# Optimization experiments

Measured on AMD Instinct MI355X. Metric: run time of the kernel, lower is better.

Reference implementation:

```python
import jax, jax.numpy as jnp
import numpy as np

B, S, E, H = 2, 2048, 1024, 16
D = E // H


def setup_inputs() -> dict:
    key = jax.random.key(0)
    ks = jax.random.split(key, 8)
    q = jax.random.normal(ks[0], (B, S, E), dtype=jnp.float32)
    k = jax.random.normal(ks[1], (B, S, E), dtype=jnp.float32)
    v = jax.random.normal(ks[2], (B, S, E), dtype=jnp.float32)
    mask = jax.random.randint(ks[3], (B, 1, 1, S), 0, 2, dtype=jnp.int32)
    sc = 1.0 / np.sqrt(E)
    W_qkv = jax.random.normal(ks[4], (3 * E, E), dtype=jnp.float32) * sc
    b_qkv = jnp.zeros((3 * E,), dtype=jnp.float32)
    W_out = jax.random.normal(ks[5], (E, E), dtype=jnp.float32) * sc
    b_out = jnp.zeros((E,), dtype=jnp.float32)
    return {"q": q, "k": k, "v": v, "mask": mask,
            "W_qkv": W_qkv, "b_qkv": b_qkv, "W_out": W_out, "b_out": b_out}


def reference(q, k, v, mask, W_qkv, b_qkv, W_out, b_out):
    # Fused qkv linear: q takes the Q-slice, k the K-slice, v the V-slice.
    qp = (q @ W_qkv[:E].T + b_qkv[:E]).reshape(B, S, H, D)
    kp = (k @ W_qkv[E:2 * E].T + b_qkv[E:2 * E]).reshape(B, S, H, D)
    vp = (v @ W_qkv[2 * E:].T + b_qkv[2 * E:]).reshape(B, S, H, D)
    # (B,H,S,S) scores -- NOTE: original module does NOT scale by sqrt(d)
    energy = jnp.einsum('nqhd,nkhd->nhqk', qp, kp)
    energy = jnp.where(mask == 0, jnp.float32(-1e20), energy)
    attention = jax.nn.softmax(energy, axis=-1)
    out = jnp.einsum('nhql,nlhd->nqhd', attention, vp).reshape(B, S, E)
    return out @ W_out.T + b_out
```

## Files before the change

### kernel.cpp

```cpp
#include <hip/hip_runtime.h>
#include <stdint.h>

constexpr int B_ = 2, S_ = 2048, E_ = 1024, H_ = 16, D_ = 64;
constexpr int M_ = B_ * S_;

typedef unsigned short u16;
typedef __attribute__((ext_vector_type(8))) short short8;
typedef __attribute__((ext_vector_type(4))) float f32x4;

__device__ __forceinline__ u16 f2bf(float f) {
  uint32_t u = __float_as_uint(f);
  return (u16)((u + 0x7FFFu + ((u >> 16) & 1u)) >> 16);
}
__device__ __forceinline__ void tsplit(float x, u16& hi, u16& lo) {
  const uint32_t u = __float_as_uint(x);
  hi = (u16)(u >> 16);
  const float hif = __uint_as_float(u & 0xFFFF0000u);
  lo = (u16)(__float_as_uint(x - hif) >> 16);
}

__device__ __forceinline__ void block_sync() {
  asm volatile("s_waitcnt lgkmcnt(0)" ::: "memory");
  __builtin_amdgcn_s_barrier();
}

typedef const __attribute__((address_space(1))) unsigned int GU32;
typedef __attribute__((address_space(3))) unsigned int LU32;
__device__ __forceinline__ void gload16(const void* g, void* l) {
  __builtin_amdgcn_global_load_lds((GU32*)g, (LU32*)l, 16, 0, 0);
}

__global__ __launch_bounds__(256) void split_f32_kernel(
    const float* __restrict__ src, u16* __restrict__ hi, u16* __restrict__ lo, int n4)
{
  const int i = blockIdx.x * 256 + threadIdx.x;
  if (i >= n4) return;
  const float4 x = ((const float4*)src)[i];
  ushort4 h, l;
  tsplit(x.x, h.x, l.x); tsplit(x.y, h.y, l.y);
  tsplit(x.z, h.z, l.z); tsplit(x.w, h.w, l.w);
  ((ushort4*)hi)[i] = h;
  ((ushort4*)lo)[i] = l;
}

__global__ __launch_bounds__(256) void mask_scan_kernel(
    const int* __restrict__ mask, int* __restrict__ opos, int* __restrict__ nk)
{
  __shared__ int tmp[256];
  __shared__ int coff;
  const int b = blockIdx.x, t = threadIdx.x;
  for (int c = t; c < S_; c += 256) opos[b * S_ + c] = 0;
  if (t == 0) coff = 0;
  __syncthreads();
  for (int c = 0; c < S_; c += 256) {
    const int m = (mask[b * S_ + c + t] != 0) ? 1 : 0;
    int x = m;
    tmp[t] = x;
    __syncthreads();
#pragma unroll
    for (int off = 1; off < 256; off <<= 1) {
      const int v = (t >= off) ? tmp[t - off] : 0;
      __syncthreads();
      x += v;
      tmp[t] = x;
      __syncthreads();
    }
    const int base = coff;
    if (m) opos[b * S_ + base + x - 1] = c + t;
    __syncthreads();
    if (t == 255) coff = base + x;
    __syncthreads();
  }
  if (t == 0) nk[b] = coff;
}

__global__ __launch_bounds__(256) void gemm_qkv_kernel(
    const float* __restrict__ q, const float* __restrict__ k, const float* __restrict__ v,
    const u16* __restrict__ WHi, const u16* __restrict__ WLo,
    const float* __restrict__ bias,
    const int* __restrict__ Opos, const int* __restrict__ NkArr,
    u16* __restrict__ QpHi, u16* __restrict__ QpLo,
    u16* __restrict__ KpHi, u16* __restrict__ KpLo,
    u16* __restrict__ Vp)
{
  __shared__ __align__(16) short smem[18432];
  short* Ah = smem;
  short* Al = smem + 5120;
  short* Bh = smem + 10240;
  short* Bl = smem + 14336;

  const int t = threadIdx.x;
  const int m0 = blockIdx.x * 128;
  const int n0g = blockIdx.y * 128;
  const int proj = n0g >> 10;
  const int nloc = n0g & (E_ - 1);
  const bool split = (proj < 2);
  const int bb = m0 >> 11, mloc = m0 & (S_ - 1);
  const int nkb = NkArr[bb];
  if (proj != 0 && mloc >= nkb) return;

  const float* A = (proj == 0) ? q : (proj == 1) ? k : v;

  const int w = t >> 6, lane = t & 63;
  const int g = lane >> 4, lc = lane & 15;
  const int wm = w & 1, wn = w >> 1;
  const int sra = t >> 1, sca = (t & 1) * 16;

  int arow;
  if (proj == 0) arow = m0 + sra;
  else arow = bb * S_ + (Opos[bb * S_ + mloc + sra] & (S_ - 1));
  const float* Ab = A + (size_t)arow * E_ + sca;

  f32x4 acc[4][4];
#pragma unroll
  for (int i = 0; i < 4; ++i)
#pragma unroll
    for (int j = 0; j < 4; ++j) acc[i][j] = (f32x4){0.f, 0.f, 0.f, 0.f};

  auto loadA = [&](float4* a, int kk) {
#pragma unroll
    for (int i = 0; i < 4; ++i) a[i] = *(const float4*)(Ab + kk + 4 * i);
  };
  auto writeA = [&](const float4* a) {
    ushort hh[16], ll[16];
#pragma unroll
    for (int i = 0; i < 4; ++i) {
      tsplit(a[i].x, hh[4 * i + 0], ll[4 * i + 0]);
      tsplit(a[i].y, hh[4 * i + 1], ll[4 * i + 1]);
      tsplit(a[i].z, hh[4 * i + 2], ll[4 * i + 2]);
      tsplit(a[i].w, hh[4 * i + 3], ll[4 * i + 3]);
    }
    *(short8*)&Ah[sra * 40 + sca]     = *(const short8*)&hh[0];
    *(short8*)&Ah[sra * 40 + sca + 8] = *(const short8*)&hh[8];
    if (split) {
      *(short8*)&Al[sra * 40 + sca]     = *(const short8*)&ll[0];
      *(short8*)&Al[sra * 40 + sca + 8] = *(const short8*)&ll[8];
    }
  };
  auto gloadB = [&](int k0) {
#pragma unroll
    for (int i = 0; i < 2; ++i) {
      const int c = (w * 2 + i) * 64 + lane;
      const int row = c >> 2;
      const int sub = (c & 3) ^ ((row >> 1) & 3);
      const size_t go = (size_t)(n0g + row) * E_ + k0 + sub * 8;
      gload16(WHi + go, (char*)Bh + (w * 2 + i) * 1024);
      if (split) gload16(WLo + go, (char*)Bl + (w * 2 + i) * 1024);
    }
  };

  float4 ar[4];
  loadA(ar, 0);

  for (int k0 = 0; k0 < E_; k0 += 32) {
    __syncthreads();
    writeA(ar);
    gloadB(k0);
    __syncthreads();
    if (k0 + 32 < E_) loadA(ar, k0 + 32);

    short8 ah[4], al[4], bh[4], bl[4];
#pragma unroll
    for (int mt = 0; mt < 4; ++mt) {
      const int ro = (wm * 64 + mt * 16 + lc) * 40 + g * 8;
      ah[mt] = *(const short8*)&Ah[ro];
      if (split) al[mt] = *(const short8*)&Al[ro];
    }
#pragma unroll
    for (int nt = 0; nt < 4; ++nt) {
      const int row = wn * 64 + nt * 16 + lc;
      const int ro = row * 32 + ((g ^ ((row >> 1) & 3)) * 8);
      bh[nt] = *(const short8*)&Bh[ro];
      if (split) bl[nt] = *(const short8*)&Bl[ro];
    }
#pragma unroll
    for (int mt = 0; mt < 4; ++mt)
#pragma unroll
      for (int nt = 0; nt < 4; ++nt) {
        f32x4 a = acc[mt][nt];
        a = __builtin_amdgcn_mfma_f32_16x16x32_bf16(ah[mt], bh[nt], a, 0, 0, 0);
        if (split) {
          a = __builtin_amdgcn_mfma_f32_16x16x32_bf16(ah[mt], bl[nt], a, 0, 0, 0);
          a = __builtin_amdgcn_mfma_f32_16x16x32_bf16(al[mt], bh[nt], a, 0, 0, 0);
        }
        acc[mt][nt] = a;
      }
  }

  float bs[4];
#pragma unroll
  for (int nt = 0; nt < 4; ++nt) bs[nt] = bias[n0g + wn * 64 + nt * 16 + lc];

  if (proj < 2) {
    u16* Hi = (proj == 0) ? QpHi : KpHi;
    u16* Lo = (proj == 0) ? QpLo : KpLo;
    const int hwave = (nloc + wn * 64) >> 6;
    short* T = smem + w * 4608;
    const int srow_out = (proj == 0) ? ((m0 + wm * 64 + lane) & (S_ - 1))
                                     : (mloc + wm * 64 + lane);
    const size_t rowb = (((size_t)(bb * H_ + hwave)) * S_ + srow_out) * D_;
#pragma unroll
    for (int pass = 0; pass < 2; ++pass) {
      __syncthreads();
#pragma unroll
      for (int nt = 0; nt < 4; ++nt)
#pragma unroll
        for (int mt = 0; mt < 4; ++mt)
#pragma unroll
          for (int r = 0; r < 4; ++r) {
            const float val = acc[mt][nt][r] + bs[nt];
            const uint32_t u = __float_as_uint(val);
            u16 x;
            if (pass == 0) x = (u16)(u >> 16);
            else {
              const float hif = __uint_as_float(u & 0xFFFF0000u);
              x = (u16)(__float_as_uint(val - hif) >> 16);
            }
            T[(mt * 16 + g * 4 + r) * 72 + nt * 16 + lc] = (short)x;
          }
      __syncthreads();
      u16* dst = (pass == 0) ? Hi : Lo;
#pragma unroll
      for (int j = 0; j < 8; ++j)
        *(short8*)&dst[rowb + 8 * j] = *(const short8*)&T[lane * 72 + 8 * j];
    }
  } else {
#pragma unroll
    for (int mt = 0; mt < 4; ++mt) {
      const int jb = mloc + wm * 64 + mt * 16 + g * 4;
#pragma unroll
      for (int nt = 0; nt < 4; ++nt) {
        const int nE = nloc + wn * 64 + nt * 16 + lc;
        const int h = nE >> 6, d = nE & 63;
        const size_t rb = (((size_t)(bb * H_ + h)) * D_ + d) * S_;
#pragma unroll
        for (int r = 0; r < 4; ++r) {
          if (jb + r < nkb) Vp[rb + jb + r] = f2bf(acc[mt][nt][r] + bs[nt]);
        }
      }
    }
  }
}

__global__ __launch_bounds__(256, 4) void attn_mfma_kernel(
    const u16* __restrict__ QpHi, const u16* __restrict__ QpLo,
    const u16* __restrict__ KpHi, const u16* __restrict__ KpLo,
    const u16* __restrict__ Vp,
    const int* __restrict__ nkArr,
    u16* __restrict__ AOHi)
{
  __shared__ __align__(16) short sm[18432];
  short* Khi = sm;
  short* Klo = sm + 4608;
  short* Vt  = sm + 9216;
  short* Pb  = sm + 13824;

  const int t = threadIdx.x;
  const int w = t >> 6, lane = t & 63;
  const int g = lane >> 4, lc = lane & 15;
  const int bh = blockIdx.y;
  const int b = bh >> 4, hh = bh & 15;
  const int q0 = blockIdx.x * 64;
  const size_t hb = (size_t)bh * S_ * D_;
  const u16* QgH = QpHi + hb;
  const u16* QgL = QpLo + hb;
  const u16* KgH = KpHi + hb;
  const u16* KgL = KpLo + hb;
  const u16* Vg  = Vp + hb;
  short* Pw = Pb + w * 1152;

  const int nk = nkArr[b];
  const int kend = ((nk + 63) >> 6) << 6;

  short8 qh[2], ql[2];
  {
    const size_t base = (size_t)(q0 + 16 * w + lc) * D_ + 8 * g;
    qh[0] = *(const short8*)&QgH[base];
    qh[1] = *(const short8*)&QgH[base + 32];
    ql[0] = *(const short8*)&QgL[base];
    ql[1] = *(const short8*)&QgL[base + 32];
  }

  short8 ones8 = {0, 0, 0, 0, 0, 0, 0, 0};
  if (lc == 0) {
    const short o = (short)0x3F80;
    ones8 = (short8){o, o, o, o, o, o, o, o};
  }

  f32x4 O[4];
  f32x4 Ol = (f32x4){0.f, 0.f, 0.f, 0.f};
#pragma unroll
  for (int dt = 0; dt < 4; ++dt) O[dt] = (f32x4){0.f, 0.f, 0.f, 0.f};
  float mst[4] = {-INFINITY, -INFINITY, -INFINITY, -INFINITY};

  const int srow = t >> 2, sc16 = (t & 3) * 16;

  short8 kr[2], lr[2], vr[2];
  kr[0] = *(const short8*)&KgH[srow * D_ + sc16];
  kr[1] = *(const short8*)&KgH[srow * D_ + sc16 + 8];
  lr[0] = *(const short8*)&KgL[srow * D_ + sc16];
  lr[1] = *(const short8*)&KgL[srow * D_ + sc16 + 8];
  vr[0] = *(const short8*)&Vg[srow * S_ + sc16];
  vr[1] = *(const short8*)&Vg[srow * S_ + sc16 + 8];

  for (int kt = 0; kt < kend; kt += 64) {
    block_sync();
    *(short8*)&Khi[srow * 72 + sc16]     = kr[0];
    *(short8*)&Khi[srow * 72 + sc16 + 8] = kr[1];
    *(short8*)&Klo[srow * 72 + sc16]     = lr[0];
    *(short8*)&Klo[srow * 72 + sc16 + 8] = lr[1];
    *(short8*)&Vt[srow * 72 + sc16]      = vr[0];
    *(short8*)&Vt[srow * 72 + sc16 + 8]  = vr[1];
    block_sync();
    if (kt + 64 < kend) {
      const int kn = kt + 64;
      kr[0] = *(const short8*)&KgH[(kn + srow) * D_ + sc16];
      kr[1] = *(const short8*)&KgH[(kn + srow) * D_ + sc16 + 8];
      lr[0] = *(const short8*)&KgL[(kn + srow) * D_ + sc16];
      lr[1] = *(const short8*)&KgL[(kn + srow) * D_ + sc16 + 8];
      vr[0] = *(const short8*)&Vg[srow * S_ + kn + sc16];
      vr[1] = *(const short8*)&Vg[srow * S_ + kn + sc16 + 8];
    }

    f32x4 sc[4];
#pragma unroll
    for (int kt16 = 0; kt16 < 4; ++kt16) {
      const int ko = (16 * kt16 + lc) * 72 + 8 * g;
      const short8 kh0 = *(const short8*)&Khi[ko];
      const short8 kh1 = *(const short8*)&Khi[ko + 32];
      const short8 kl0 = *(const short8*)&Klo[ko];
      const short8 kl1 = *(const short8*)&Klo[ko + 32];
      f32x4 a = {0.f, 0.f, 0.f, 0.f};
      a = __builtin_amdgcn_mfma_f32_16x16x32_bf16(qh[0], kh0, a, 0, 0, 0);
      a = __builtin_amdgcn_mfma_f32_16x16x32_bf16(qh[1], kh1, a, 0, 0, 0);
      a = __builtin_amdgcn_mfma_f32_16x16x32_bf16(qh[0], kl0, a, 0, 0, 0);
      a = __builtin_amdgcn_mfma_f32_16x16x32_bf16(qh[1], kl1, a, 0, 0, 0);
      a = __builtin_amdgcn_mfma_f32_16x16x32_bf16(ql[0], kh0, a, 0, 0, 0);
      a = __builtin_amdgcn_mfma_f32_16x16x32_bf16(ql[1], kh1, a, 0, 0, 0);
      sc[kt16] = a;
    }

    if (kt + 64 > nk) {
#pragma unroll
      for (int kt16 = 0; kt16 < 4; ++kt16) {
        if (kt + 16 * kt16 + lc >= nk) {
          sc[kt16][0] = -1e20f; sc[kt16][1] = -1e20f;
          sc[kt16][2] = -1e20f; sc[kt16][3] = -1e20f;
        }
      }
    }

    float al[4];
#pragma unroll
    for (int r = 0; r < 4; ++r) {
      float vv = fmaxf(fmaxf(sc[0][r], sc[1][r]), fmaxf(sc[2][r], sc[3][r]));
      vv = fmaxf(vv, __shfl_xor(vv, 1));
      vv = fmaxf(vv, __shfl_xor(vv, 2));
      vv = fmaxf(vv, __shfl_xor(vv, 4));
      vv = fmaxf(vv, __shfl_xor(vv, 8));
      const float mn = fmaxf(mst[r], vv);
      al[r] = __expf(mst[r] - mn);
      mst[r] = mn;
    }
#pragma unroll
    for (int kt16 = 0; kt16 < 4; ++kt16) {
#pragma unroll
      for (int r = 0; r < 4; ++r)
        sc[kt16][r] = __expf(sc[kt16][r] - mst[r]);
    }
    const f32x4 alv = {al[0], al[1], al[2], al[3]};
    O[0] *= alv; O[1] *= alv; O[2] *= alv; O[3] *= alv;
    Ol *= alv;
#pragma unroll
    for (int kt16 = 0; kt16 < 4; ++kt16) {
#pragma unroll
      for (int r = 0; r < 4; ++r)
        Pw[(4 * g + r) * 72 + 16 * kt16 + lc] = (short)f2bf(sc[kt16][r]);
    }

    short8 pa[2];
    pa[0] = *(const short8*)&Pw[lc * 72 + 8 * g];
    pa[1] = *(const short8*)&Pw[lc * 72 + 32 + 8 * g];
    Ol = __builtin_amdgcn_mfma_f32_16x16x32_bf16(pa[0], ones8, Ol, 0, 0, 0);
    Ol = __builtin_amdgcn_mfma_f32_16x16x32_bf16(pa[1], ones8, Ol, 0, 0, 0);
#pragma unroll
    for (int dt = 0; dt < 4; ++dt) {
      const int vo = (16 * dt + lc) * 72 + 8 * g;
      const short8 vb0 = *(const short8*)&Vt[vo];
      const short8 vb1 = *(const short8*)&Vt[vo + 32];
      O[dt] = __builtin_amdgcn_mfma_f32_16x16x32_bf16(pa[0], vb0, O[dt], 0, 0, 0);
      O[dt] = __builtin_amdgcn_mfma_f32_16x16x32_bf16(pa[1], vb1, O[dt], 0, 0, 0);
    }
  }

#pragma unroll
  for (int r = 0; r < 4; ++r) {
    const float lv = __shfl(Ol[r], lane & 48);
    const float lir = 1.0f / lv;
    const int qrow = q0 + 16 * w + 4 * g + r;
    const size_t rowb = (size_t)(b * S_ + qrow) * E_ + hh * 64;
#pragma unroll
    for (int dt = 0; dt < 4; ++dt)
      AOHi[rowb + dt * 16 + lc] = f2bf(O[dt][r] * lir);
  }
}

__global__ __launch_bounds__(256) void gemm_out_kernel(
    const u16* __restrict__ AHi,
    const u16* __restrict__ WHi,
    const float* __restrict__ bias, float* __restrict__ out)
{
  __shared__ __align__(16) short smem[6144];
  short* Ah = smem;
  short* Bh = smem + 2048;

  const int t = threadIdx.x;
  const int m0 = blockIdx.x * 64;
  const int n0 = blockIdx.y * 128;
  const int w = t >> 6, lane = t & 63;
  const int g = lane >> 4, lc = lane & 15;
  const int wm = w & 1, wn = w >> 1;

  f32x4 acc[2][4];
#pragma unroll
  for (int i = 0; i < 2; ++i)
#pragma unroll
    for (int j = 0; j < 4; ++j) acc[i][j] = (f32x4){0.f, 0.f, 0.f, 0.f};

  for (int k0 = 0; k0 < E_; k0 += 32) {
    {
      const int cA = w * 64 + lane;
      const int rowA = cA >> 2;
      const int subA = (cA & 3) ^ ((rowA >> 1) & 3);
      gload16(AHi + (size_t)(m0 + rowA) * E_ + k0 + subA * 8,
              (char*)Ah + w * 1024);
#pragma unroll
      for (int i = 0; i < 2; ++i) {
        const int c = (w * 2 + i) * 64 + lane;
        const int row = c >> 2;
        const int sub = (c & 3) ^ ((row >> 1) & 3);
        gload16(WHi + (size_t)(n0 + row) * E_ + k0 + sub * 8,
                (char*)Bh + (w * 2 + i) * 1024);
      }
    }
    __syncthreads();

    short8 ah[2], bh[4];
#pragma unroll
    for (int mt = 0; mt < 2; ++mt) {
      const int row = wm * 32 + mt * 16 + lc;
      ah[mt] = *(const short8*)&Ah[row * 32 + ((g ^ ((row >> 1) & 3)) * 8)];
    }
#pragma unroll
    for (int nt = 0; nt < 4; ++nt) {
      const int row = wn * 64 + nt * 16 + lc;
      bh[nt] = *(const short8*)&Bh[row * 32 + ((g ^ ((row >> 1) & 3)) * 8)];
    }
#pragma unroll
    for (int mt = 0; mt < 2; ++mt)
#pragma unroll
      for (int nt = 0; nt < 4; ++nt)
        acc[mt][nt] = __builtin_amdgcn_mfma_f32_16x16x32_bf16(ah[mt], bh[nt], acc[mt][nt], 0, 0, 0);
    __syncthreads();
  }

  float bs[4];
#pragma unroll
  for (int nt = 0; nt < 4; ++nt) bs[nt] = bias[n0 + wn * 64 + nt * 16 + lc];
#pragma unroll
  for (int nt = 0; nt < 4; ++nt) {
    const int nc = n0 + wn * 64 + nt * 16 + lc;
#pragma unroll
    for (int mt = 0; mt < 2; ++mt) {
#pragma unroll
      for (int r = 0; r < 4; ++r) {
        const int mrow = m0 + wm * 32 + mt * 16 + g * 4 + r;
        out[(size_t)mrow * E_ + nc] = acc[mt][nt][r] + bs[nt];
      }
    }
  }
}

extern "C" void kernel_launch(void* const* d_in, const int* in_sizes, int n_in,
                              void* d_out, int out_size, void* d_ws, size_t ws_size,
                              hipStream_t stream) {
  const float* q    = (const float*)d_in[0];
  const float* k    = (const float*)d_in[1];
  const float* v    = (const float*)d_in[2];
  const int*   mask = (const int*)d_in[3];
  const float* Wqkv = (const float*)d_in[4];
  const float* bqkv = (const float*)d_in[5];
  const float* Wout = (const float*)d_in[6];
  const float* bout = (const float*)d_in[7];
  float* out = (float*)d_out;

  char* wsb = (char*)d_ws;
  u16* WqkvHi = (u16*)(wsb + 0);
  u16* WqkvLo = (u16*)(wsb + 6291456);
  u16* WoutHi = (u16*)(wsb + 12582912);
  int* Opos   = (int*)(wsb + 14680064);
  int* Nk     = (int*)(wsb + 14680064 + 16384);
  u16* WoutLo = (u16*)(wsb + 14680064);
  u16* QpHi   = (u16*)(wsb + 16777216);
  u16* QpLo   = (u16*)(wsb + 25165824);
  u16* KpHi   = (u16*)(wsb + 33554432);
  u16* KpLo   = (u16*)(wsb + 41943040);
  u16* Vp     = (u16*)(wsb + 50331648);
  u16* AOHi   = (u16*)(wsb + 58720256);

  hipLaunchKernelGGL(split_f32_kernel, dim3(3072), dim3(256), 0, stream,
                     Wqkv, WqkvHi, WqkvLo, 786432);
  hipLaunchKernelGGL(split_f32_kernel, dim3(1024), dim3(256), 0, stream,
                     Wout, WoutHi, WoutLo, 262144);
  hipLaunchKernelGGL(mask_scan_kernel, dim3(B_), dim3(256), 0, stream,
                     mask, Opos, Nk);
  hipMemsetAsync(Vp, 0, 8388608, stream);
  hipLaunchKernelGGL(gemm_qkv_kernel, dim3(M_ / 128, 24), dim3(256), 0, stream,
                     q, k, v, WqkvHi, WqkvLo, bqkv, Opos, Nk,
                     QpHi, QpLo, KpHi, KpLo, Vp);
  hipLaunchKernelGGL(attn_mfma_kernel, dim3(S_ / 64, B_ * H_), dim3(256), 0, stream,
                     QpHi, QpLo, KpHi, KpLo, Vp, Nk, AOHi);
  hipLaunchKernelGGL(gemm_out_kernel, dim3(M_ / 64, E_ / 128), dim3(256), 0, stream,
                     AOHi, WoutHi, bout, out);
}
```

Baseline: 266.4 us.

## Use direct global-to-LDS loads with XOR swizzle in QKV GEMM and attention

In the QKV projection GEMM, the fp32 A tile is no longer loaded into registers and split into bf16 hi/lo before the LDS write. It is now copied straight into LDS as fp32 via global_load_lds with an XOR-swizzled layout, and each wave splits it into hi/lo when it reads its MFMA operands. The attention kernel likewise drops register prefetching of K/V and instead issues global_load_lds into swizzled, unpadded LDS tiles each iteration. This cuts VGPR use and LDS store instructions. In exchange it loses the overlap between register prefetch and compute, since each load is now issued and waited on inside the same iteration, and the hi/lo split work is repeated by every wave that reads a row.

```diff
diff --git a/kernel.cpp b/kernel.cpp
--- a/kernel.cpp
+++ b/kernel.cpp
@@ -17,11 +17,6 @@
   hi = (u16)(u >> 16);
   const float hif = __uint_as_float(u & 0xFFFF0000u);
   lo = (u16)(__float_as_uint(x - hif) >> 16);
-}
-
-__device__ __forceinline__ void block_sync() {
-  asm volatile("s_waitcnt lgkmcnt(0)" ::: "memory");
-  __builtin_amdgcn_s_barrier();
 }
 
 typedef const __attribute__((address_space(1))) unsigned int GU32;
@@ -84,10 +79,9 @@
     u16* __restrict__ Vp)
 {
   __shared__ __align__(16) short smem[18432];
-  short* Ah = smem;
-  short* Al = smem + 5120;
-  short* Bh = smem + 10240;
-  short* Bl = smem + 14336;
+  float* Af = (float*)smem;
+  short* Bh = smem + 8192;
+  short* Bl = smem + 12288;
 
   const int t = threadIdx.x;
   const int m0 = blockIdx.x * 128;
@@ -104,39 +98,17 @@
   const int w = t >> 6, lane = t & 63;
   const int g = lane >> 4, lc = lane & 15;
   const int wm = w & 1, wn = w >> 1;
-  const int sra = t >> 1, sca = (t & 1) * 16;
-
-  int arow;
-  if (proj == 0) arow = m0 + sra;
-  else arow = bb * S_ + (Opos[bb * S_ + mloc + sra] & (S_ - 1));
-  const float* Ab = A + (size_t)arow * E_ + sca;
-
-  f32x4 acc[4][4];
-#pragma unroll
-  for (int i = 0; i < 4; ++i)
-#pragma unroll
-    for (int j = 0; j < 4; ++j) acc[i][j] = (f32x4){0.f, 0.f, 0.f, 0.f};
-
-  auto loadA = [&](float4* a, int kk) {
-#pragma unroll
-    for (int i = 0; i < 4; ++i) a[i] = *(const float4*)(Ab + kk + 4 * i);
-  };
-  auto writeA = [&](const float4* a) {
-    ushort hh[16], ll[16];
-#pragma unroll
-    for (int i = 0; i < 4; ++i) {
-      tsplit(a[i].x, hh[4 * i + 0], ll[4 * i + 0]);
-      tsplit(a[i].y, hh[4 * i + 1], ll[4 * i + 1]);
-      tsplit(a[i].z, hh[4 * i + 2], ll[4 * i + 2]);
-      tsplit(a[i].w, hh[4 * i + 3], ll[4 * i + 3]);
-    }
-    *(short8*)&Ah[sra * 40 + sca]     = *(const short8*)&hh[0];
-    *(short8*)&Ah[sra * 40 + sca + 8] = *(const short8*)&hh[8];
-    if (split) {
-      *(short8*)&Al[sra * 40 + sca]     = *(const short8*)&ll[0];
-      *(short8*)&Al[sra * 40 + sca + 8] = *(const short8*)&ll[8];
-    }
-  };
+
+  const int lchA = (lane & 7) ^ (lane >> 3);
+  const float* Asrc[4];
+#pragma unroll
+  for (int i = 0; i < 4; ++i) {
+    const int r = (i * 4 + w) * 8 + (lane >> 3);
+    int ga;
+    if (proj == 0) ga = m0 + r;
+    else ga = bb * S_ + (Opos[bb * S_ + mloc + r] & (S_ - 1));
+    Asrc[i] = A + (size_t)ga * E_ + 4 * lchA;
+  }
   auto gloadB = [&](int k0) {
 #pragma unroll
     for (int i = 0; i < 2; ++i) {
@@ -149,22 +121,33 @@
     }
   };
 
-  float4 ar[4];
-  loadA(ar, 0);
+  f32x4 acc[4][4];
+#pragma unroll
+  for (int i = 0; i < 4; ++i)
+#pragma unroll
+    for (int j = 0; j < 4; ++j) acc[i][j] = (f32x4){0.f, 0.f, 0.f, 0.f};
 
   for (int k0 = 0; k0 < E_; k0 += 32) {
     __syncthreads();
-    writeA(ar);
+#pragma unroll
+    for (int i = 0; i < 4; ++i)
+      gload16(Asrc[i] + k0, (char*)Af + (i * 4 + w) * 1024);
     gloadB(k0);
     __syncthreads();
-    if (k0 + 32 < E_) loadA(ar, k0 + 32);
 
     short8 ah[4], al[4], bh[4], bl[4];
 #pragma unroll
     for (int mt = 0; mt < 4; ++mt) {
-      const int ro = (wm * 64 + mt * 16 + lc) * 40 + g * 8;
-      ah[mt] = *(const short8*)&Ah[ro];
-      if (split) al[mt] = *(const short8*)&Al[ro];
+      const int R = wm * 64 + mt * 16 + lc;
+      const int s = lc & 7;
+      const float4 f0 = *(const float4*)&Af[R * 32 + ((2 * g) ^ s) * 4];
+      const float4 f1 = *(const float4*)&Af[R * 32 + ((2 * g + 1) ^ s) * 4];
+      const float xs[8] = {f0.x, f0.y, f0.z, f0.w, f1.x, f1.y, f1.z, f1.w};
+      ushort hh[8], ll[8];
+#pragma unroll
+      for (int j = 0; j < 8; ++j) tsplit(xs[j], hh[j], ll[j]);
+      ah[mt] = *(const short8*)&hh[0];
+      if (split) al[mt] = *(const short8*)&ll[0];
     }
 #pragma unroll
     for (int nt = 0; nt < 4; ++nt) {
@@ -249,11 +232,11 @@
     const int* __restrict__ nkArr,
     u16* __restrict__ AOHi)
 {
-  __shared__ __align__(16) short sm[18432];
+  __shared__ __align__(16) short sm[16896];
   short* Khi = sm;
-  short* Klo = sm + 4608;
-  short* Vt  = sm + 9216;
-  short* Pb  = sm + 13824;
+  short* Klo = sm + 4096;
+  short* Vt  = sm + 8192;
+  short* Pb  = sm + 12288;
 
   const int t = threadIdx.x;
   const int w = t >> 6, lane = t & 63;
@@ -293,43 +276,35 @@
   for (int dt = 0; dt < 4; ++dt) O[dt] = (f32x4){0.f, 0.f, 0.f, 0.f};
   float mst[4] = {-INFINITY, -INFINITY, -INFINITY, -INFINITY};
 
-  const int srow = t >> 2, sc16 = (t & 3) * 16;
-
-  short8 kr[2], lr[2], vr[2];
-  kr[0] = *(const short8*)&KgH[srow * D_ + sc16];
-  kr[1] = *(const short8*)&KgH[srow * D_ + sc16 + 8];
-  lr[0] = *(const short8*)&KgL[srow * D_ + sc16];
-  lr[1] = *(const short8*)&KgL[srow * D_ + sc16 + 8];
-  vr[0] = *(const short8*)&Vg[srow * S_ + sc16];
-  vr[1] = *(const short8*)&Vg[srow * S_ + sc16 + 8];
+  const int lch = (lane & 7) ^ (lane >> 3);
+  int grow[2];
+#pragma unroll
+  for (int i = 0; i < 2; ++i) grow[i] = (i * 4 + w) * 8 + (lane >> 3);
 
   for (int kt = 0; kt < kend; kt += 64) {
-    block_sync();
-    *(short8*)&Khi[srow * 72 + sc16]     = kr[0];
-    *(short8*)&Khi[srow * 72 + sc16 + 8] = kr[1];
-    *(short8*)&Klo[srow * 72 + sc16]     = lr[0];
-    *(short8*)&Klo[srow * 72 + sc16 + 8] = lr[1];
-    *(short8*)&Vt[srow * 72 + sc16]      = vr[0];
-    *(short8*)&Vt[srow * 72 + sc16 + 8]  = vr[1];
-    block_sync();
-    if (kt + 64 < kend) {
-      const int kn = kt + 64;
-      kr[0] = *(const short8*)&KgH[(kn + srow) * D_ + sc16];
-      kr[1] = *(const short8*)&KgH[(kn + srow) * D_ + sc16 + 8];
-      lr[0] = *(const short8*)&KgL[(kn + srow) * D_ + sc16];
-      lr[1] = *(const short8*)&KgL[(kn + srow) * D_ + sc16 + 8];
-      vr[0] = *(const short8*)&Vg[srow * S_ + kn + sc16];
-      vr[1] = *(const short8*)&Vg[srow * S_ + kn + sc16 + 8];
-    }
+    __syncthreads();
+#pragma unroll
+    for (int i = 0; i < 2; ++i) {
+      const int row = grow[i];
+      const size_t ko = (size_t)(kt + row) * D_ + lch * 8;
+      gload16(KgH + ko, (char*)Khi + (i * 4 + w) * 1024);
+      gload16(KgL + ko, (char*)Klo + (i * 4 + w) * 1024);
+      gload16(Vg + (size_t)row * S_ + kt + lch * 8,
+              (char*)Vt + (i * 4 + w) * 1024);
+    }
+    __syncthreads();
 
     f32x4 sc[4];
 #pragma unroll
     for (int kt16 = 0; kt16 < 4; ++kt16) {
-      const int ko = (16 * kt16 + lc) * 72 + 8 * g;
-      const short8 kh0 = *(const short8*)&Khi[ko];
-      const short8 kh1 = *(const short8*)&Khi[ko + 32];
-      const short8 kl0 = *(const short8*)&Klo[ko];
-      const short8 kl1 = *(const short8*)&Klo[ko + 32];
+      const int R = 16 * kt16 + lc;
+      const int s = lc & 7;
+      const int o0 = R * 64 + ((g ^ s)) * 8;
+      const int o1 = R * 64 + (((g + 4) ^ s)) * 8;
+      const short8 kh0 = *(const short8*)&Khi[o0];
+      const short8 kh1 = *(const short8*)&Khi[o1];
+      const short8 kl0 = *(const short8*)&Klo[o0];
+      const short8 kl1 = *(const short8*)&Klo[o1];
       f32x4 a = {0.f, 0.f, 0.f, 0.f};
       a = __builtin_amdgcn_mfma_f32_16x16x32_bf16(qh[0], kh0, a, 0, 0, 0);
       a = __builtin_amdgcn_mfma_f32_16x16x32_bf16(qh[1], kh1, a, 0, 0, 0);
@@ -385,9 +360,10 @@
     Ol = __builtin_amdgcn_mfma_f32_16x16x32_bf16(pa[1], ones8, Ol, 0, 0, 0);
 #pragma unroll
     for (int dt = 0; dt < 4; ++dt) {
-      const int vo = (16 * dt + lc) * 72 + 8 * g;
-      const short8 vb0 = *(const short8*)&Vt[vo];
-      const short8 vb1 = *(const short8*)&Vt[vo + 32];
+      const int R = 16 * dt + lc;
+      const int s = lc & 7;
+      const short8 vb0 = *(const short8*)&Vt[R * 64 + ((g ^ s)) * 8];
+      const short8 vb1 = *(const short8*)&Vt[R * 64 + (((g + 4) ^ s)) * 8];
       O[dt] = __builtin_amdgcn_mfma_f32_16x16x32_bf16(pa[0], vb0, O[dt], 0, 0, 0);
       O[dt] = __builtin_amdgcn_mfma_f32_16x16x32_bf16(pa[1], vb1, O[dt], 0, 0, 0);
     }
```

Measured after the change: 308.0 us. 15.6% more time.
